# Optimization experiments

Hardware: AMD Instinct MI355X
Metric: run time of the kernel (lower is better)

## Reference

```python
import jax, jax.numpy as jnp
import numpy as np

B, T, C = 64, 2048, 32
OUT_T = 2048

def setup_inputs() -> dict:
    key = jax.random.key(0)
    k1, k2 = jax.random.split(key)
    X = jax.random.normal(k1, (B, T, C), dtype=jnp.float32)
    # small init so deformations are modest displacements, like a trained locnet
    W_loc = jax.random.normal(k2, (T * C, OUT_T), dtype=jnp.float32) * 1e-3
    b_loc = jnp.zeros((OUT_T,), dtype=jnp.float32)
    return {"X": X, "W_loc": W_loc, "b_loc": b_loc}

def reference(X, W_loc, b_loc):
    b, t, c = X.shape
    out_t = W_loc.shape[1]
    # localization net: flatten + dense -> per-output-point displacement (B, OUT_T)
    deformation = X.reshape(b, t * c) @ W_loc + b_loc
    # sampling grid: linspace(0, T-1, OUT_T), shared across batch, shifted by deformation
    grid = jnp.linspace(0.0, jnp.float32(t - 1), out_t)  # (OUT_T,)
    x = grid[None, :] + deformation                       # (B, OUT_T) float sample coords
    # linear interpolation with clamped integer neighbors
    x0 = jnp.floor(x).astype(jnp.int32)
    x1 = x0 + 1
    x0c = jnp.clip(x0, 0, t - 1)
    x1c = jnp.clip(x1, 0, t - 1)
    batch_idx = jnp.arange(b)[:, None]                    # (B, 1)
    v0 = X[batch_idx, x0c]                                # (B, OUT_T, C) gather along T
    v1 = X[batch_idx, x1c]                                # (B, OUT_T, C)
    # weights use the CLIPPED coords cast back to float (faithful to original)
    w0 = (x1c.astype(x.dtype) - x)[..., None]             # (B, OUT_T, 1)
    w1 = (x - x0c.astype(x.dtype))[..., None]
    return w0 * v0 + w1 * v1                              # (B, OUT_T, C)
```

## Files before the change

### kernel.cpp

```cpp
#include <hip/hip_runtime.h>
#include <hip/hip_bf16.h>
#include <stdint.h>

constexpr int BATCH = 64;
constexpr int T     = 2048;
constexpr int CCH   = 32;
constexpr int OUT_T = 2048;
constexpr int K     = T * CCH;
constexpr int N     = OUT_T;

constexpr int TN     = 64;
constexpr int KSPLIT = 64;
constexpr int CK     = K / KSPLIT;
constexpr int BK     = 32;

typedef __attribute__((ext_vector_type(8))) short short8;
typedef __attribute__((ext_vector_type(4))) float f32x4;

__device__ __forceinline__ void split_bf16(float x, ushort& h, ushort& l) {
  unsigned xb = __float_as_uint(x);
  h = (ushort)(xb >> 16);
  float hf = __uint_as_float(xb & 0xFFFF0000u);
  float lf = x - hf;
  unsigned u = __float_as_uint(lf);
  unsigned r = u + 0x7FFFu + ((u >> 16) & 1u);
  l = (ushort)(r >> 16);
}

__global__ __launch_bounds__(256) void gemm_split_kernel(
    const float* __restrict__ X,
    const float* __restrict__ W,
    float* __restrict__ def) {
  const int bn = blockIdx.x % (N / TN);
  const int bk = blockIdx.x / (N / TN);
  const int tid  = threadIdx.x;
  const int lane = tid & 63;
  const int wave = tid >> 6;
  const int r = lane & 15;
  const int g = lane >> 4;

  __shared__ ushort Ahi[64][32];
  __shared__ ushort Alo[64][32];
  __shared__ ushort Bhi[64][40];
  __shared__ ushort Blo[64][40];

  f32x4 acc[4] = {};

  const int kbase = bk * CK;

  for (int ks = 0; ks < CK / BK; ++ks) {
    const int k0 = kbase + ks * BK;

    __syncthreads();

#pragma unroll
    for (int it = 0; it < 2; ++it) {
      int flat = it * 256 + tid;
      int m  = flat >> 3;
      int kq = flat & 7;
      const float4 v = *(const float4*)&X[(size_t)m * K + k0 + kq * 4];
      ushort h0, h1, h2, h3, l0, l1, l2, l3;
      split_bf16(v.x, h0, l0); split_bf16(v.y, h1, l1);
      split_bf16(v.z, h2, l2); split_bf16(v.w, h3, l3);
      uint2 ph; ph.x = (unsigned)h0 | ((unsigned)h1 << 16);
                ph.y = (unsigned)h2 | ((unsigned)h3 << 16);
      uint2 pl; pl.x = (unsigned)l0 | ((unsigned)l1 << 16);
                pl.y = (unsigned)l2 | ((unsigned)l3 << 16);
      *(uint2*)&Ahi[m][kq * 4] = ph;
      *(uint2*)&Alo[m][kq * 4] = pl;
    }

#pragma unroll
    for (int it = 0; it < 2; ++it) {
      int flat = it * 256 + tid;
      int n  = flat & 63;
      int kq = flat >> 6;
      float v0 = W[(size_t)(k0 + kq * 4 + 0) * N + bn * TN + n];
      float v1 = W[(size_t)(k0 + kq * 4 + 1) * N + bn * TN + n];
      float v2 = W[(size_t)(k0 + kq * 4 + 2) * N + bn * TN + n];
      float v3 = W[(size_t)(k0 + kq * 4 + 3) * N + bn * TN + n];
      ushort h0, h1, h2, h3, l0, l1, l2, l3;
      split_bf16(v0, h0, l0); split_bf16(v1, h1, l1);
      split_bf16(v2, h2, l2); split_bf16(v3, h3, l3);
      uint2 ph; ph.x = (unsigned)h0 | ((unsigned)h1 << 16);
                ph.y = (unsigned)h2 | ((unsigned)h3 << 16);
      uint2 pl; pl.x = (unsigned)l0 | ((unsigned)l1 << 16);
                pl.y = (unsigned)l2 | ((unsigned)l3 << 16);
      *(uint2*)&Bhi[n][kq * 4] = ph;
      *(uint2*)&Blo[n][kq * 4] = pl;
    }

    __syncthreads();

    short8 bh = *(const short8*)&Bhi[wave * 16 + r][g * 8];
    short8 bl = *(const short8*)&Blo[wave * 16 + r][g * 8];
#pragma unroll
    for (int mf = 0; mf < 4; ++mf) {
      short8 ah = *(const short8*)&Ahi[mf * 16 + r][g * 8];
      short8 al = *(const short8*)&Alo[mf * 16 + r][g * 8];
      acc[mf] = __builtin_amdgcn_mfma_f32_16x16x32_bf16(ah, bh, acc[mf], 0, 0, 0);
      acc[mf] = __builtin_amdgcn_mfma_f32_16x16x32_bf16(ah, bl, acc[mf], 0, 0, 0);
      acc[mf] = __builtin_amdgcn_mfma_f32_16x16x32_bf16(al, bh, acc[mf], 0, 0, 0);
    }
  }

  const int ncol = bn * TN + wave * 16 + r;
#pragma unroll
  for (int mf = 0; mf < 4; ++mf) {
    const int mbase = mf * 16 + g * 4;
#pragma unroll
    for (int q = 0; q < 4; ++q) {
      atomicAdd(&def[(size_t)(mbase + q) * N + ncol], acc[mf][q]);
    }
  }
}

__global__ __launch_bounds__(256) void resample_kernel(
    const float* __restrict__ X,
    const float* __restrict__ def,
    const float* __restrict__ b_loc,
    float* __restrict__ out) {
  const int tid = blockIdx.x * 256 + threadIdx.x;
  const int c4 = tid & 7;
  const int o  = (tid >> 3) & (OUT_T - 1);
  const int b  = tid >> 14;

  const float x = (float)o + def[b * OUT_T + o] + b_loc[o];
  const float xf = floorf(x);
  const int x0 = (int)xf;
  const int x1 = x0 + 1;
  const int x0c = min(max(x0, 0), T - 1);
  const int x1c = min(max(x1, 0), T - 1);
  const float w0 = (float)x1c - x;
  const float w1 = x - (float)x0c;

  const float4 v0 = *(const float4*)&X[((size_t)b * T + x0c) * CCH + c4 * 4];
  const float4 v1 = *(const float4*)&X[((size_t)b * T + x1c) * CCH + c4 * 4];
  float4 res;
  res.x = w0 * v0.x + w1 * v1.x;
  res.y = w0 * v0.y + w1 * v1.y;
  res.z = w0 * v0.z + w1 * v1.z;
  res.w = w0 * v0.w + w1 * v1.w;
  *(float4*)&out[((size_t)b * OUT_T + o) * CCH + c4 * 4] = res;
}

extern "C" void kernel_launch(void* const* d_in, const int* in_sizes, int n_in,
                              void* d_out, int out_size, void* d_ws, size_t ws_size,
                              hipStream_t stream) {
  const float* X     = (const float*)d_in[0];
  const float* W     = (const float*)d_in[1];
  const float* b_loc = (const float*)d_in[2];
  float* out = (float*)d_out;
  float* def = (float*)d_ws;

  hipMemsetAsync(def, 0, (size_t)BATCH * N * sizeof(float), stream);

  dim3 gblk((N / TN) * KSPLIT);
  gemm_split_kernel<<<gblk, 256, 0, stream>>>(X, W, def);

  dim3 rblk((BATCH * OUT_T * 8) / 256);
  resample_kernel<<<rblk, 256, 0, stream>>>(X, def, b_loc, out);
}
```

Measured before the change: 722.2 us.

## Double-buffer LDS tiles with register prefetch and remap block order in split-K GEMM

The GEMM main loop now prefetches the next K-slice of X and W into registers while MFMAs run on the current LDS buffer, then converts and stores into the alternate buffer. This removes one barrier per iteration and hides global load latency behind compute. Block indices are also remapped with (bid&7)*256+(bid>>3) so consecutive blocks land on different XCD-style groups, which changes L2 locality. The cost is doubled LDS and more registers, which could lower occupancy.

```diff
diff --git a/kernel.cpp b/kernel.cpp
--- a/kernel.cpp
+++ b/kernel.cpp
@@ -10,9 +10,11 @@
 constexpr int N     = OUT_T;
 
 constexpr int TN     = 64;
+constexpr int NBN    = N / TN;
 constexpr int KSPLIT = 64;
 constexpr int CK     = K / KSPLIT;
 constexpr int BK     = 32;
+constexpr int NS     = CK / BK;
 
 typedef __attribute__((ext_vector_type(8))) short short8;
 typedef __attribute__((ext_vector_type(4))) float f32x4;
@@ -31,34 +33,58 @@
     const float* __restrict__ X,
     const float* __restrict__ W,
     float* __restrict__ def) {
-  const int bn = blockIdx.x % (N / TN);
-  const int bk = blockIdx.x / (N / TN);
+  const int bid = blockIdx.x;
+  const int lb  = (bid & 7) * 256 + (bid >> 3);
+  const int bn  = lb & (NBN - 1);
+  const int bk  = lb >> 5;
+
   const int tid  = threadIdx.x;
   const int lane = tid & 63;
   const int wave = tid >> 6;
   const int r = lane & 15;
   const int g = lane >> 4;
 
-  __shared__ ushort Ahi[64][32];
-  __shared__ ushort Alo[64][32];
-  __shared__ ushort Bhi[64][40];
-  __shared__ ushort Blo[64][40];
+  __shared__ ushort Ahi[2][64][32];
+  __shared__ ushort Alo[2][64][32];
+  __shared__ ushort Bhi[2][64][40];
+  __shared__ ushort Blo[2][64][40];
 
   f32x4 acc[4] = {};
 
   const int kbase = bk * CK;
 
-  for (int ks = 0; ks < CK / BK; ++ks) {
+  float4 aReg[2];
+  float  bReg[2][4];
+
+  auto issue_loads = [&](int ks) {
     const int k0 = kbase + ks * BK;
-
-    __syncthreads();
-
 #pragma unroll
     for (int it = 0; it < 2; ++it) {
       int flat = it * 256 + tid;
       int m  = flat >> 3;
       int kq = flat & 7;
-      const float4 v = *(const float4*)&X[(size_t)m * K + k0 + kq * 4];
+      aReg[it] = *(const float4*)&X[(size_t)m * K + k0 + kq * 4];
+    }
+#pragma unroll
+    for (int it = 0; it < 2; ++it) {
+      int flat = it * 256 + tid;
+      int n  = flat & 63;
+      int kq = flat >> 6;
+      const float* wp = &W[(size_t)(k0 + kq * 4) * N + bn * TN + n];
+      bReg[it][0] = wp[0];
+      bReg[it][1] = wp[N];
+      bReg[it][2] = wp[2 * N];
+      bReg[it][3] = wp[3 * N];
+    }
+  };
+
+  auto stage = [&](int buf) {
+#pragma unroll
+    for (int it = 0; it < 2; ++it) {
+      int flat = it * 256 + tid;
+      int m  = flat >> 3;
+      int kq = flat & 7;
+      const float4 v = aReg[it];
       ushort h0, h1, h2, h3, l0, l1, l2, l3;
       split_bf16(v.x, h0, l0); split_bf16(v.y, h1, l1);
       split_bf16(v.z, h2, l2); split_bf16(v.w, h3, l3);
@@ -66,42 +92,47 @@
                 ph.y = (unsigned)h2 | ((unsigned)h3 << 16);
       uint2 pl; pl.x = (unsigned)l0 | ((unsigned)l1 << 16);
                 pl.y = (unsigned)l2 | ((unsigned)l3 << 16);
-      *(uint2*)&Ahi[m][kq * 4] = ph;
-      *(uint2*)&Alo[m][kq * 4] = pl;
+      *(uint2*)&Ahi[buf][m][kq * 4] = ph;
+      *(uint2*)&Alo[buf][m][kq * 4] = pl;
     }
-
 #pragma unroll
     for (int it = 0; it < 2; ++it) {
       int flat = it * 256 + tid;
       int n  = flat & 63;
       int kq = flat >> 6;
-      float v0 = W[(size_t)(k0 + kq * 4 + 0) * N + bn * TN + n];
-      float v1 = W[(size_t)(k0 + kq * 4 + 1) * N + bn * TN + n];
-      float v2 = W[(size_t)(k0 + kq * 4 + 2) * N + bn * TN + n];
-      float v3 = W[(size_t)(k0 + kq * 4 + 3) * N + bn * TN + n];
       ushort h0, h1, h2, h3, l0, l1, l2, l3;
-      split_bf16(v0, h0, l0); split_bf16(v1, h1, l1);
-      split_bf16(v2, h2, l2); split_bf16(v3, h3, l3);
+      split_bf16(bReg[it][0], h0, l0); split_bf16(bReg[it][1], h1, l1);
+      split_bf16(bReg[it][2], h2, l2); split_bf16(bReg[it][3], h3, l3);
       uint2 ph; ph.x = (unsigned)h0 | ((unsigned)h1 << 16);
                 ph.y = (unsigned)h2 | ((unsigned)h3 << 16);
       uint2 pl; pl.x = (unsigned)l0 | ((unsigned)l1 << 16);
                 pl.y = (unsigned)l2 | ((unsigned)l3 << 16);
-      *(uint2*)&Bhi[n][kq * 4] = ph;
-      *(uint2*)&Blo[n][kq * 4] = pl;
+      *(uint2*)&Bhi[buf][n][kq * 4] = ph;
+      *(uint2*)&Blo[buf][n][kq * 4] = pl;
     }
+  };
 
-    __syncthreads();
+  issue_loads(0);
+  stage(0);
+  __syncthreads();
 
-    short8 bh = *(const short8*)&Bhi[wave * 16 + r][g * 8];
-    short8 bl = *(const short8*)&Blo[wave * 16 + r][g * 8];
+  for (int ks = 0; ks < NS; ++ks) {
+    const int cur = ks & 1;
+    if (ks + 1 < NS) issue_loads(ks + 1);
+
+    short8 bh = *(const short8*)&Bhi[cur][wave * 16 + r][g * 8];
+    short8 bl = *(const short8*)&Blo[cur][wave * 16 + r][g * 8];
 #pragma unroll
     for (int mf = 0; mf < 4; ++mf) {
-      short8 ah = *(const short8*)&Ahi[mf * 16 + r][g * 8];
-      short8 al = *(const short8*)&Alo[mf * 16 + r][g * 8];
+      short8 ah = *(const short8*)&Ahi[cur][mf * 16 + r][g * 8];
+      short8 al = *(const short8*)&Alo[cur][mf * 16 + r][g * 8];
       acc[mf] = __builtin_amdgcn_mfma_f32_16x16x32_bf16(ah, bh, acc[mf], 0, 0, 0);
       acc[mf] = __builtin_amdgcn_mfma_f32_16x16x32_bf16(ah, bl, acc[mf], 0, 0, 0);
       acc[mf] = __builtin_amdgcn_mfma_f32_16x16x32_bf16(al, bh, acc[mf], 0, 0, 0);
     }
+
+    if (ks + 1 < NS) stage(cur ^ 1);
+    __syncthreads();
   }
 
   const int ncol = bn * TN + wave * 16 + r;
@@ -155,7 +186,7 @@
 
   hipMemsetAsync(def, 0, (size_t)BATCH * N * sizeof(float), stream);
 
-  dim3 gblk((N / TN) * KSPLIT);
+  dim3 gblk(NBN * KSPLIT);
   gemm_split_kernel<<<gblk, 256, 0, stream>>>(X, W, def);
 
   dim3 rblk((BATCH * OUT_T * 8) / 256);
```

After: 709.2 us. About the same (-1.8%).
